# Performance work log

Measured on AMD Instinct MI355X. Metric: run time of the kernel, lower is better.

Reference implementation:

```python
import jax, jax.numpy as jnp
import numpy as np

B, NUM_OBJECTS, NUM_ATTRS, T = 8, 128, 4, 12
MAX_CONCEPTS, EMBED_DIM, IDENTITY_DIM, ATTENTION_DIM, HIDDEN_DIM = 2048, 128, 64, 64, 256
OP_MODE, OP_INSERT, OP_TRANSFER = 0, 1, 2


def setup_inputs() -> dict:
    key = jax.random.key(0)
    ks = jax.random.split(key, 24)
    def rn(k, shape, s=0.05):
        return s * jax.random.normal(k, shape, dtype=jnp.float32)
    return {
        'scene': jax.random.randint(ks[0], (B, NUM_OBJECTS, NUM_ATTRS), 0, MAX_CONCEPTS - 1),
        'program_op': jax.random.randint(ks[1], (B, T), 0, 3),
        'program_arg': jax.random.randint(ks[2], (B, T), 0, MAX_CONCEPTS),
        'attr_emb_in': rn(ks[3], (MAX_CONCEPTS, EMBED_DIM)),
        'attr_emb_out': rn(ks[4], (MAX_CONCEPTS, EMBED_DIM)),
        'attr_emb_id': rn(ks[5], (MAX_CONCEPTS, IDENTITY_DIM)),
        'concept_emb_in': rn(ks[6], (MAX_CONCEPTS, EMBED_DIM)),
        'concept_emb_out': rn(ks[7], (MAX_CONCEPTS, EMBED_DIM)),
        'concept_emb_id': rn(ks[8], (MAX_CONCEPTS, IDENTITY_DIM)),
        'embed_init': rn(ks[9], (EMBED_DIM,)),
        'identity_init': rn(ks[10], (IDENTITY_DIM,)),
        'attention_init': jnp.zeros((ATTENTION_DIM,), dtype=jnp.float32),
        'axon_w1': rn(ks[11], (HIDDEN_DIM, ATTENTION_DIM + IDENTITY_DIM)),
        'axon_b1': rn(ks[12], (HIDDEN_DIM,)),
        'axon_w2': rn(ks[13], (ATTENTION_DIM, HIDDEN_DIM)),
        'axon_b2': rn(ks[14], (ATTENTION_DIM,)),
        'meta_w1': rn(ks[15], (HIDDEN_DIM, EMBED_DIM + ATTENTION_DIM)),
        'meta_b1': rn(ks[16], (HIDDEN_DIM,)),
        'meta_w2': rn(ks[17], (ATTENTION_DIM, HIDDEN_DIM)),
        'meta_b2': rn(ks[18], (ATTENTION_DIM,)),
    }


def _mlp(x, w1, b1, w2, b2):
    # torch Linear convention: y = x @ W.T + b
    return jnp.maximum(x @ w1.T + b1, 0.0) @ w2.T + b2


def reference(scene, program_op, program_arg, attr_emb_in, attr_emb_out, attr_emb_id,
              concept_emb_in, concept_emb_out, concept_emb_id,
              embed_init, identity_init, attention_init,
              axon_w1, axon_b1, axon_w2, axon_b2,
              meta_w1, meta_b1, meta_w2, meta_b2):
    Bq, N, _ = scene.shape
    C = MAX_CONCEPTS + N  # dim_concept
    mask = (scene != -1).astype(jnp.float32)  # (B,N,A) non-background mask
    def embed_bg(E):
        return (E[scene + 1] * mask[..., None]).sum(2)  # (B,N,D)
    objects_in = embed_bg(attr_emb_in)
    objects_out = embed_bg(attr_emb_out)
    objects_id = embed_bg(attr_emb_id)

    rep = lambda w: jnp.broadcast_to(w[None], (Bq,) + w.shape)
    dendron = jnp.concatenate([rep(concept_emb_in), objects_in], 1)    # (B,C,E)
    axon = jnp.concatenate([rep(concept_emb_out), objects_out], 1)     # (B,C,E)
    identity = jnp.concatenate([rep(concept_emb_id), objects_id], 1)   # (B,C,Id)
    weight_matrix = jnp.einsum('bie,bje->bij', dendron, axon)           # (B,C,C)

    arguments = concept_emb_out[program_arg]                            # (B,T,E)
    is_mode = (program_op == OP_MODE).astype(jnp.float32)               # (B,T)
    is_insert = (program_op == OP_INSERT).astype(jnp.float32)
    is_transfer = (program_op == OP_TRANSFER).astype(jnp.float32)

    meta0 = jnp.broadcast_to(attention_init[None], (Bq, ATTENTION_DIM))
    att0 = jnp.broadcast_to(attention_init[None, None], (Bq, C, ATTENTION_DIM))

    def step(carry, xs):
        meta, attention = carry
        arg_i, m, ins, tr = xs  # (B,E), (B,), (B,), (B,)
        new_meta = _mlp(jnp.concatenate([meta, arg_i], 1), meta_w1, meta_b1, meta_w2, meta_b2)
        meta = m[:, None] * new_meta + (1.0 - m[:, None]) * meta
        # (arguments * axon).mean over embed dim -> (B,C)
        proj = jnp.einsum('be,bce->bc', arg_i, axon) / EMBED_DIM
        attention_insert = meta[:, None, :] * proj[:, :, None]          # (B,C,A)
        attended_weight = weight_matrix * attention.mean(2)[:, None, :] # (B,C,C)
        ia = jnp.concatenate([identity, attention], 2)                  # (B,C,Id+A)
        # (attended_weight[:,:,:,None] * ia[:,None]).mean(2) == matmul / C
        gathered = jnp.einsum('bij,bjd->bid', attended_weight, ia) / C  # (B,C,Id+A)
        attention_transfer = _mlp(gathered, axon_w1, axon_b1, axon_w2, axon_b2) + gathered[..., IDENTITY_DIM:]
        attention = attention + ins[:, None, None] * attention_insert + tr[:, None, None] * attention_transfer
        attention = jnp.clip(jnp.where(attention >= 0, attention, 0.01 * attention), -1.0, 2.0)
        return (meta, attention), (attention, attention_insert, attention_transfer)

    xs = (jnp.swapaxes(arguments, 0, 1), is_mode.T, is_insert.T, is_transfer.T)
    (meta, attention), (att_hist, ins_hist, trans_hist) = jax.lax.scan(step, (meta0, att0), xs)
    output_softmax = jax.nn.log_softmax(attention.mean(2), axis=1)  # (B,C)
    return (output_softmax, att_hist, ins_hist, trans_hist)
```

## Files before the change

### kernel.cpp

```cpp
#include <hip/hip_runtime.h>

#define B 8
#define NOBJ 128
#define NATTR 4
#define T 12
#define MC 2048
#define E 128
#define IDD 64
#define AD 64
#define HD 256
#define C 2176

typedef short s16x8 __attribute__((ext_vector_type(8)));
typedef float f32x4 __attribute__((ext_vector_type(4)));

__device__ inline unsigned short f2b(float f) {
  union { float f; unsigned u; } v; v.f = f;
  unsigned r = v.u + 0x7FFFu + ((v.u >> 16) & 1u);
  return (unsigned short)(r >> 16);
}
__device__ inline float b2f(unsigned short u) {
  union { unsigned u; float f; } v; v.u = ((unsigned)u) << 16;
  return v.f;
}

__device__ __forceinline__ void st_coh_u64(unsigned long long* p, unsigned long long v) {
  __hip_atomic_store(p, v, __ATOMIC_RELAXED, __HIP_MEMORY_SCOPE_AGENT);
}
__device__ __forceinline__ unsigned long long ld_coh_u64(const unsigned long long* p) {
  return __hip_atomic_load(p, __ATOMIC_RELAXED, __HIP_MEMORY_SCOPE_AGENT);
}
__device__ __forceinline__ void st_coh_u32(unsigned* p, unsigned v) {
  __hip_atomic_store(p, v, __ATOMIC_RELAXED, __HIP_MEMORY_SCOPE_AGENT);
}
__device__ __forceinline__ unsigned ld_coh_u32(const unsigned* p) {
  return __hip_atomic_load(p, __ATOMIC_RELAXED, __HIP_MEMORY_SCOPE_AGENT);
}

__device__ __forceinline__ int gidx(int r, int c) {
  return r * 128 + ((((c >> 3) ^ (r & 15)) << 3) | (c & 7));
}
__device__ __forceinline__ int hidx(int r, int c) {
  return r * 256 + ((((c >> 3) ^ (r & 15)) << 3) | (c & 7));
}
__device__ __forceinline__ int mtidx(int r, int c) {
  return r * 128 + ((((c >> 3) ^ (r & 15)) << 3) | (c & 7));
}

__global__ __launch_bounds__(256) void k_setup1(
    const int* __restrict__ scene,
    const float* __restrict__ aein, const float* __restrict__ aeout,
    const float* __restrict__ aeid,
    const float* __restrict__ cein, const float* __restrict__ ceout,
    const float* __restrict__ ceid,
    const float* __restrict__ aw1, const float* __restrict__ aw2,
    const float* __restrict__ mw1, const float* __restrict__ mw2,
    unsigned short* __restrict__ dendron_bf, float* __restrict__ axon,
    float* __restrict__ identity,
    unsigned short* __restrict__ w1_bf, unsigned short* __restrict__ w2_bf,
    float* __restrict__ mw1T, float* __restrict__ mw2T,
    unsigned* __restrict__ mflag) {
  int blk = blockIdx.x;
  int tid = threadIdx.x;
  if (blk < 4352) {
    int gid = blk * 2 + (tid >> 7);
    int e = tid & 127;
    int b = gid / C, j = gid % C;
    float din, dout, did = 0.f;
    if (j < MC) {
      din  = cein[j * E + e];
      dout = ceout[j * E + e];
      if (e < IDD) did = ceid[j * IDD + e];
    } else {
      int obj = j - MC;
      float sIn = 0.f, sOut = 0.f, sId = 0.f;
      for (int a = 0; a < NATTR; a++) {
        int s = scene[(b * NOBJ + obj) * NATTR + a];
        float m = (s != -1) ? 1.f : 0.f;
        int idx = s + 1;
        sIn  += aein[idx * E + e] * m;
        sOut += aeout[idx * E + e] * m;
        if (e < IDD) sId += aeid[idx * IDD + e] * m;
      }
      din = sIn; dout = sOut; did = sId;
    }
    dendron_bf[(size_t)gid * E + e] = f2b(din);
    axon[(size_t)gid * E + e] = dout;
    if (e < IDD) identity[(size_t)gid * IDD + e] = did;
  } else if (blk < 4544) {
    int i = (blk - 4352) * 256 + tid;
    if (i < HD * E)  w1_bf[i] = f2b(aw1[i]);
    if (i < AD * HD) w2_bf[i] = f2b(aw2[i]);
    if (i < 192 * HD) { int c = i / HD, k = i % HD; mw1T[c * HD + k] = mw1[k * 192 + c]; }
    if (i < HD * AD)  { int k = i / AD, a = i % AD; mw2T[k * AD + a] = mw2[a * HD + k]; }
  } else {
    if (tid < B * 16) mflag[tid] = 0u;
  }
}

__global__ __launch_bounds__(256) void k_setup2(
    const float* __restrict__ axon, const float* __restrict__ identity,
    const float* __restrict__ att_init,
    const int* __restrict__ prog_op, const int* __restrict__ prog_arg,
    const float* __restrict__ ceout,
    const float* __restrict__ mw1T, const float* __restrict__ mb1,
    const float* __restrict__ mw2T, const float* __restrict__ mb2,
    unsigned short* __restrict__ axonT, unsigned short* __restrict__ idT_g,
    unsigned short* __restrict__ siaT, float* __restrict__ att_g,
    float* __restrict__ meta_all, float* __restrict__ proj_all) {
  int blk = blockIdx.x;
  int tid = threadIdx.x;
  if (blk < 272) {
    int b = blk / 34, jc = blk % 34;
    int j0 = jc * 64;
    __shared__ float ax[64][129];
    __shared__ float idb[64][65];
    int lane = tid & 63, lr = lane & 15;
    float s = att_init[lane];
    s += __shfl_xor(s, 1, 64);  s += __shfl_xor(s, 2, 64);
    s += __shfl_xor(s, 4, 64);  s += __shfl_xor(s, 8, 64);
    s += __shfl_xor(s, 16, 64); s += __shfl_xor(s, 32, 64);
    float am0 = s * (1.f / AD);
    for (int i = tid; i < 64 * 128; i += 256) {
      int j = i >> 7, e = i & 127;
      ax[j][e] = axon[(size_t)(b * C + j0 + j) * E + e];
    }
    for (int i = tid; i < 64 * 64; i += 256) {
      int j = i >> 6, d = i & 63;
      idb[j][d] = identity[(size_t)(b * C + j0 + j) * IDD + d];
    }
    __syncthreads();
    for (int i = tid; i < 128 * 64; i += 256) {
      int e = i >> 6, jj = i & 63;
      axonT[(size_t)(b * E + e) * C + j0 + jj] = f2b(ax[jj][e]);
    }
    for (int i = tid; i < 64 * 64; i += 256) {
      int d = i >> 6, jj = i & 63;
      idT_g[(size_t)(b * 64 + d) * C + j0 + jj] = f2b(idb[jj][d]);
      siaT[(size_t)(b * 128 + d) * C + j0 + jj] = f2b(idb[jj][d] * am0);
      siaT[(size_t)(b * 128 + 64 + d) * C + j0 + jj] = f2b(att_init[d] * am0);
    }
    {
      float* ag = att_g + (size_t)blk * 4096 + tid * 16;
      #pragma unroll
      for (int n = 0; n < 4; n++) {
        float v0 = att_init[n * 16 + lr];
        #pragma unroll
        for (int v = 0; v < 4; v++) ag[n * 4 + v] = v0;
      }
    }
  } else if (blk < 280) {
    int b = blk - 272;
    __shared__ float x[192];
    __shared__ float h[HD];
    __shared__ float meta[AD];
    if (tid < AD) meta[tid] = att_init[tid];
    __syncthreads();
    for (int t = 0; t < T; t++) {
      int arg = prog_arg[b * T + t];
      if (tid < AD) x[tid] = meta[tid];
      else if (tid < 192) x[tid] = ceout[arg * E + (tid - 64)];
      __syncthreads();
      float s = mb1[tid];
      for (int c = 0; c < 192; c++) s += x[c] * mw1T[c * HD + tid];
      h[tid] = fmaxf(s, 0.f);
      __syncthreads();
      if (tid < AD) {
        float o = mb2[tid];
        for (int k = 0; k < HD; k++) o += h[k] * mw2T[k * AD + tid];
        float m = (prog_op[b * T + t] == 0) ? 1.f : 0.f;
        float nm = m * o + (1.f - m) * meta[tid];
        meta[tid] = nm;
        meta_all[(t * B + b) * AD + tid] = nm;
      }
      __syncthreads();
    }
  } else {
    int gid = (blk - 280) * 4 + (tid >> 6);
    int lane = tid & 63;
    int b = gid / C, i = gid % C;
    float a0 = axon[(size_t)gid * E + lane];
    float a1 = axon[(size_t)gid * E + 64 + lane];
    for (int t = 0; t < T; t++) {
      int arg = prog_arg[b * T + t];
      float p = a0 * ceout[arg * E + lane] + a1 * ceout[arg * E + 64 + lane];
      for (int off = 1; off < 64; off <<= 1) p += __shfl_xor(p, off, 64);
      if (lane == 0) proj_all[(size_t)(t * B + b) * C + i] = p * (1.f / E);
    }
  }
}

__global__ __launch_bounds__(256) void k_step(
    int t,
    const unsigned short* __restrict__ dendron_bf,
    const unsigned short* __restrict__ axonT,
    const unsigned short* __restrict__ idT_g,
    const unsigned short* __restrict__ siaT_in,
    const unsigned short* __restrict__ w1_bf, const float* __restrict__ b1g,
    const unsigned short* __restrict__ w2_bf, const float* __restrict__ b2g,
    const float* __restrict__ proj_all, const float* __restrict__ meta_all,
    const int* __restrict__ prog_op,
    unsigned long long* __restrict__ Mt64,
    float* __restrict__ att_g, unsigned short* __restrict__ siaT_out,
    float* __restrict__ rowmean,
    float* __restrict__ att_hist, float* __restrict__ ins_hist,
    float* __restrict__ trans_hist,
    unsigned* __restrict__ mflag) {
  const int blk = blockIdx.x;
  const int b = blk / 34, ch = blk % 34, j0 = ch * 64;
  const int tid = threadIdx.x;
  const int w = tid >> 6, lane = tid & 63, lr = lane & 15, lg = lane >> 4;

  __shared__ unsigned short smem[24576];
  __shared__ float am_l[64];
  unsigned short* g_l = smem;
  unsigned short* mt  = smem + 8192;
  unsigned short* h_l = smem + 8192;
  float* mred = (float*)smem;

  const f32x4 z = {0.f, 0.f, 0.f, 0.f};
  const unsigned ph = (unsigned)(t + 1);

  float att[4][4];
  {
    const f32x4* ag = (const f32x4*)(att_g + (size_t)blk * 4096 + tid * 16);
    #pragma unroll
    for (int n = 0; n < 4; n++) {
      f32x4 v4 = ag[n];
      #pragma unroll
      for (int v = 0; v < 4; v++) att[n][v] = v4[v];
    }
  }

  if (ch < 16) {
    int d0 = (ch >> 2) * 32, e0 = (ch & 3) * 32;
    const unsigned short* ap0 = siaT_in + (size_t)(b * 128 + d0 + lr) * C + w * 544 + lg * 8;
    const unsigned short* ap1 = ap0 + (size_t)16 * C;
    const unsigned short* bp0 = axonT + (size_t)(b * E + e0 + lr) * C + w * 544 + lg * 8;
    const unsigned short* bp1 = bp0 + (size_t)16 * C;
    f32x4 a00 = z, a01 = z, a10 = z, a11 = z;
    #pragma unroll 4
    for (int kk = 0; kk < 17; kk++) {
      int k0 = kk * 32;
      s16x8 A0 = *(const s16x8*)(ap0 + k0);
      s16x8 A1 = *(const s16x8*)(ap1 + k0);
      s16x8 B0 = *(const s16x8*)(bp0 + k0);
      s16x8 B1 = *(const s16x8*)(bp1 + k0);
      a00 = __builtin_amdgcn_mfma_f32_16x16x32_bf16(A0, B0, a00, 0, 0, 0);
      a01 = __builtin_amdgcn_mfma_f32_16x16x32_bf16(A0, B1, a01, 0, 0, 0);
      a10 = __builtin_amdgcn_mfma_f32_16x16x32_bf16(A1, B0, a10, 0, 0, 0);
      a11 = __builtin_amdgcn_mfma_f32_16x16x32_bf16(A1, B1, a11, 0, 0, 0);
    }
    #pragma unroll
    for (int v = 0; v < 4; v++) {
      mred[(w * 32 + lg * 4 + v) * 33 + lr]          = a00[v];
      mred[(w * 32 + lg * 4 + v) * 33 + 16 + lr]     = a01[v];
      mred[(w * 32 + 16 + lg * 4 + v) * 33 + lr]     = a10[v];
      mred[(w * 32 + 16 + lg * 4 + v) * 33 + 16 + lr] = a11[v];
    }
    __syncthreads();
    {
      int r = tid >> 3, c = (tid & 7) * 4;
      float s0 = 0.f, s1 = 0.f, s2 = 0.f, s3 = 0.f;
      #pragma unroll
      for (int w4 = 0; w4 < 4; w4++) {
        const float* p = &mred[(w4 * 32 + r) * 33 + c];
        s0 += p[0]; s1 += p[1]; s2 += p[2]; s3 += p[3];
      }
      unsigned long long pk = (unsigned long long)f2b(s0)
                            | ((unsigned long long)f2b(s1) << 16)
                            | ((unsigned long long)f2b(s2) << 32)
                            | ((unsigned long long)f2b(s3) << 48);
      st_coh_u64(Mt64 + (((size_t)(b * 128 + d0 + r) * 128) + e0 + c) / 4, pk);
    }
    asm volatile("s_waitcnt vmcnt(0)" ::: "memory");
    __syncthreads();
    if (tid == 0) st_coh_u32(mflag + b * 16 + ch, ph);
  }
  if (tid < 16) {
    while (ld_coh_u32(mflag + b * 16 + tid) < ph) __builtin_amdgcn_s_sleep(1);
  }
  __syncthreads();
  {
    const unsigned long long* mtp = Mt64 + (size_t)b * 4096;
    #pragma unroll
    for (int k = 0; k < 16; k++) {
      int idx = tid + k * 256;
      unsigned long long v = ld_coh_u64(mtp + idx);
      int r = idx >> 5, c4 = (idx & 31) * 4;
      *(unsigned long long*)&mt[mtidx(r, c4)] = v;
    }
  }
  __syncthreads();
  {
    s16x8 afr[4];
    #pragma unroll
    for (int ke = 0; ke < 4; ke++)
      afr[ke] = *(const s16x8*)(dendron_bf + (size_t)(b * C + j0 + w * 16 + lr) * E + ke * 32 + lg * 8);
    #pragma unroll
    for (int n = 0; n < 8; n++) {
      f32x4 acc = z;
      #pragma unroll
      for (int ke = 0; ke < 4; ke++) {
        s16x8 bf = *(const s16x8*)&mt[mtidx(n * 16 + lr, ke * 32 + lg * 8)];
        acc = __builtin_amdgcn_mfma_f32_16x16x32_bf16(afr[ke], bf, acc, 0, 0, 0);
      }
      #pragma unroll
      for (int v = 0; v < 4; v++)
        g_l[gidx(w * 16 + lg * 4 + v, n * 16 + lr)] = f2b(acc[v] * (1.f / C));
    }
  }
  __syncthreads();
  {
    s16x8 gf[4];
    #pragma unroll
    for (int kd = 0; kd < 4; kd++)
      gf[kd] = *(const s16x8*)&g_l[gidx(w * 16 + lr, kd * 32 + lg * 8)];
    #pragma unroll
    for (int n = 0; n < 16; n++) {
      f32x4 acc = z;
      #pragma unroll
      for (int kd = 0; kd < 4; kd++) {
        s16x8 bf = *(const s16x8*)(w1_bf + (size_t)(n * 16 + lr) * E + kd * 32 + lg * 8);
        acc = __builtin_amdgcn_mfma_f32_16x16x32_bf16(gf[kd], bf, acc, 0, 0, 0);
      }
      float b1v = b1g[n * 16 + lr];
      #pragma unroll
      for (int v = 0; v < 4; v++)
        h_l[hidx(w * 16 + lg * 4 + v, n * 16 + lr)] = f2b(fmaxf(acc[v] + b1v, 0.f));
    }
  }
  __syncthreads();
  {
    s16x8 hf[8];
    #pragma unroll
    for (int kk = 0; kk < 8; kk++)
      hf[kk] = *(const s16x8*)&h_l[hidx(w * 16 + lr, kk * 32 + lg * 8)];
    int op = prog_op[b * T + t];
    float insF = (op == 1) ? 1.f : 0.f, trF = (op == 2) ? 1.f : 0.f;
    float projv[4];
    #pragma unroll
    for (int v = 0; v < 4; v++)
      projv[v] = proj_all[(size_t)(t * B + b) * C + j0 + w * 16 + lg * 4 + v];
    #pragma unroll
    for (int n = 0; n < 4; n++) {
      f32x4 acc = z;
      #pragma unroll
      for (int kk = 0; kk < 8; kk++) {
        s16x8 bf = *(const s16x8*)(w2_bf + (size_t)(n * 16 + lr) * HD + kk * 32 + lg * 8);
        acc = __builtin_amdgcn_mfma_f32_16x16x32_bf16(hf[kk], bf, acc, 0, 0, 0);
      }
      int a = n * 16 + lr;
      float b2v = b2g[a];
      float meta_a = meta_all[(size_t)(t * B + b) * AD + a];
      #pragma unroll
      for (int v = 0; v < 4; v++) {
        int row = lg * 4 + v;
        int i = j0 + w * 16 + row;
        float transfer = acc[v] + b2v + b2f(g_l[gidx(w * 16 + row, 64 + a)]);
        float insert = meta_a * projv[v];
        float attv = att[n][v] + insF * insert + trF * transfer;
        attv = (attv >= 0.f) ? attv : 0.01f * attv;
        attv = fminf(fmaxf(attv, -1.f), 2.f);
        att[n][v] = attv;
        size_t hi = (((size_t)t * B + b) * C + i) * AD + a;
        __builtin_nontemporal_store(attv, att_hist + hi);
        __builtin_nontemporal_store(insert, ins_hist + hi);
        __builtin_nontemporal_store(transfer, trans_hist + hi);
      }
    }
  }
  float amr[4];
  {
    float s[4];
    #pragma unroll
    for (int v = 0; v < 4; v++) s[v] = att[0][v] + att[1][v] + att[2][v] + att[3][v];
    #pragma unroll
    for (int v = 0; v < 4; v++) {
      s[v] += __shfl_xor(s[v], 1, 64);
      s[v] += __shfl_xor(s[v], 2, 64);
      s[v] += __shfl_xor(s[v], 4, 64);
      s[v] += __shfl_xor(s[v], 8, 64);
      amr[v] = s[v] * (1.f / AD);
    }
    if (lr == 0) {
      #pragma unroll
      for (int v = 0; v < 4; v++) {
        am_l[w * 16 + lg * 4 + v] = amr[v];
        rowmean[(size_t)b * C + j0 + w * 16 + lg * 4 + v] = amr[v];
      }
    }
  }
  {
    f32x4* ag = (f32x4*)(att_g + (size_t)blk * 4096 + tid * 16);
    #pragma unroll
    for (int n = 0; n < 4; n++) {
      f32x4 v4;
      #pragma unroll
      for (int v = 0; v < 4; v++) v4[v] = att[n][v];
      ag[n] = v4;
      unsigned long long pk = 0;
      #pragma unroll
      for (int v = 0; v < 4; v++)
        pk |= (unsigned long long)f2b(att[n][v] * amr[v]) << (16 * v);
      *(unsigned long long*)(siaT_out + (size_t)(b * 128 + 64 + n * 16 + lr) * C + j0 + w * 16 + lg * 4) = pk;
    }
  }
  __syncthreads();
  #pragma unroll
  for (int k = 0; k < 2; k++) {
    int idx = tid + k * 256;
    int d = idx >> 3, part = idx & 7;
    int j = part * 8;
    s16x8 iv = *(const s16x8*)(idT_g + (size_t)(b * 64 + d) * C + j0 + j);
    s16x8 ov;
    #pragma unroll
    for (int m = 0; m < 8; m++)
      ov[m] = (short)f2b(b2f((unsigned short)iv[m]) * am_l[j + m]);
    *(s16x8*)(siaT_out + (size_t)(b * 128 + d) * C + j0 + j) = ov;
  }
}

__global__ void k_softmax(const float* __restrict__ rowmean, float* __restrict__ out) {
  int b = blockIdx.x;
  __shared__ float am[C];
  __shared__ float red[256];
  int tid = threadIdx.x;
  for (int i = tid; i < C; i += 256) am[i] = rowmean[(size_t)b * C + i];
  __syncthreads();
  float mx = -1e30f;
  for (int i = tid; i < C; i += 256) mx = fmaxf(mx, am[i]);
  red[tid] = mx; __syncthreads();
  for (int s = 128; s > 0; s >>= 1) { if (tid < s) red[tid] = fmaxf(red[tid], red[tid + s]); __syncthreads(); }
  mx = red[0]; __syncthreads();
  float sm = 0.f;
  for (int i = tid; i < C; i += 256) sm += expf(am[i] - mx);
  red[tid] = sm; __syncthreads();
  for (int s = 128; s > 0; s >>= 1) { if (tid < s) red[tid] += red[tid + s]; __syncthreads(); }
  float lse = logf(red[0]) + mx;
  for (int i = tid; i < C; i += 256) out[(size_t)b * C + i] = am[i] - lse;
}

extern "C" void kernel_launch(void* const* d_in, const int* in_sizes, int n_in,
                              void* d_out, int out_size, void* d_ws, size_t ws_size,
                              hipStream_t stream) {
  const int* scene     = (const int*)d_in[0];
  const int* prog_op   = (const int*)d_in[1];
  const int* prog_arg  = (const int*)d_in[2];
  const float* aein    = (const float*)d_in[3];
  const float* aeout   = (const float*)d_in[4];
  const float* aeid    = (const float*)d_in[5];
  const float* cein    = (const float*)d_in[6];
  const float* ceout   = (const float*)d_in[7];
  const float* ceid    = (const float*)d_in[8];
  const float* att_init = (const float*)d_in[11];
  const float* aw1 = (const float*)d_in[12];
  const float* ab1 = (const float*)d_in[13];
  const float* aw2 = (const float*)d_in[14];
  const float* ab2 = (const float*)d_in[15];
  const float* mw1 = (const float*)d_in[16];
  const float* mb1 = (const float*)d_in[17];
  const float* mw2 = (const float*)d_in[18];
  const float* mb2 = (const float*)d_in[19];

  char* ws = (char*)d_ws;
  size_t off = 0;
  auto carve = [&](size_t bytes) { char* p = ws + off; off += (bytes + 255) & ~(size_t)255; return p; };
  float* axon      = (float*)carve((size_t)B * C * E * 4);
  float* identity  = (float*)carve((size_t)B * C * IDD * 4);
  float* proj_all  = (float*)carve((size_t)T * B * C * 4);
  float* meta_all  = (float*)carve((size_t)T * B * AD * 4);
  float* mw1T      = (float*)carve((size_t)192 * HD * 4);
  float* mw2T      = (float*)carve((size_t)HD * AD * 4);
  float* rowmean   = (float*)carve((size_t)B * C * 4);
  float* att_g     = (float*)carve((size_t)272 * 4096 * 4);
  unsigned short* dendron_bf = (unsigned short*)carve((size_t)B * C * E * 2);
  unsigned short* axonT      = (unsigned short*)carve((size_t)B * E * C * 2);
  unsigned short* idT_g      = (unsigned short*)carve((size_t)B * 64 * C * 2);
  unsigned short* siaT       = (unsigned short*)carve((size_t)B * 128 * C * 2);
  unsigned long long* Mt64   = (unsigned long long*)carve((size_t)B * 4096 * 8);
  unsigned short* w1_bf      = (unsigned short*)carve((size_t)HD * E * 2);
  unsigned short* w2_bf      = (unsigned short*)carve((size_t)AD * HD * 2);
  unsigned*       mflag      = (unsigned*)carve(1024);

  float* out_sm     = (float*)d_out;
  float* att_hist   = out_sm + B * C;
  float* ins_hist   = att_hist + (size_t)T * B * C * AD;
  float* trans_hist = ins_hist + (size_t)T * B * C * AD;

  k_setup1<<<dim3(4545), dim3(256), 0, stream>>>(scene, aein, aeout, aeid, cein, ceout, ceid,
                                                 aw1, aw2, mw1, mw2,
                                                 dendron_bf, axon, identity,
                                                 w1_bf, w2_bf, mw1T, mw2T, mflag);
  k_setup2<<<dim3(1368), dim3(256), 0, stream>>>(axon, identity, att_init,
                                                 prog_op, prog_arg, ceout,
                                                 mw1T, mb1, mw2T, mb2,
                                                 axonT, idT_g, siaT, att_g,
                                                 meta_all, proj_all);
  for (int t = 0; t < T; t++) {
    k_step<<<dim3(272), dim3(256), 0, stream>>>(t, dendron_bf, axonT, idT_g, siaT,
                                                w1_bf, ab1, w2_bf, ab2,
                                                proj_all, meta_all, prog_op,
                                                Mt64, att_g, siaT, rowmean,
                                                att_hist, ins_hist, trans_hist, mflag);
  }
  k_softmax<<<dim3(B), dim3(256), 0, stream>>>(rowmean, out_sm);
}
```

Before: 655.4 us.

## Fuse three scan steps per launch with inter-block flag synchronization

Replaces the twelve per-step kernel launches with four launches, each running three consecutive time steps. Between steps, blocks publish their siaT slices and wait on per-batch completion flags instead of relying on kernel boundaries. Intermediate buffers are triple-buffered and attention state stays in registers across steps. This cuts launch overhead and register/global reloads, at the cost of spin-waits that need all 272 blocks co-resident and extra coherent stores.

```diff
diff --git a/kernel.cpp b/kernel.cpp
--- a/kernel.cpp
+++ b/kernel.cpp
@@ -26,9 +26,6 @@
 
 __device__ __forceinline__ void st_coh_u64(unsigned long long* p, unsigned long long v) {
   __hip_atomic_store(p, v, __ATOMIC_RELAXED, __HIP_MEMORY_SCOPE_AGENT);
-}
-__device__ __forceinline__ unsigned long long ld_coh_u64(const unsigned long long* p) {
-  return __hip_atomic_load(p, __ATOMIC_RELAXED, __HIP_MEMORY_SCOPE_AGENT);
 }
 __device__ __forceinline__ void st_coh_u32(unsigned* p, unsigned v) {
   __hip_atomic_store(p, v, __ATOMIC_RELAXED, __HIP_MEMORY_SCOPE_AGENT);
@@ -59,7 +56,7 @@
     float* __restrict__ identity,
     unsigned short* __restrict__ w1_bf, unsigned short* __restrict__ w2_bf,
     float* __restrict__ mw1T, float* __restrict__ mw2T,
-    unsigned* __restrict__ mflag) {
+    unsigned* __restrict__ flags) {
   int blk = blockIdx.x;
   int tid = threadIdx.x;
   if (blk < 4352) {
@@ -94,7 +91,7 @@
     if (i < 192 * HD) { int c = i / HD, k = i % HD; mw1T[c * HD + k] = mw1[k * 192 + c]; }
     if (i < HD * AD)  { int k = i / AD, a = i % AD; mw2T[k * AD + a] = mw2[a * HD + k]; }
   } else {
-    if (tid < B * 16) mflag[tid] = 0u;
+    for (int i = tid; i < 512; i += 256) flags[i] = 0u;
   }
 }
 
@@ -190,22 +187,24 @@
   }
 }
 
-__global__ __launch_bounds__(256) void k_step(
-    int t,
+__global__ __launch_bounds__(256, 2) void k_grp(
+    int t0,
     const unsigned short* __restrict__ dendron_bf,
     const unsigned short* __restrict__ axonT,
     const unsigned short* __restrict__ idT_g,
-    const unsigned short* __restrict__ siaT_in,
+    const unsigned short* __restrict__ sIN,
+    unsigned short* __restrict__ sM1,
+    unsigned short* __restrict__ sM2,
+    unsigned short* __restrict__ sOUT,
     const unsigned short* __restrict__ w1_bf, const float* __restrict__ b1g,
     const unsigned short* __restrict__ w2_bf, const float* __restrict__ b2g,
     const float* __restrict__ proj_all, const float* __restrict__ meta_all,
     const int* __restrict__ prog_op,
     unsigned long long* __restrict__ Mt64,
-    float* __restrict__ att_g, unsigned short* __restrict__ siaT_out,
-    float* __restrict__ rowmean,
+    float* __restrict__ att_g, float* __restrict__ rowmean,
     float* __restrict__ att_hist, float* __restrict__ ins_hist,
     float* __restrict__ trans_hist,
-    unsigned* __restrict__ mflag) {
+    unsigned* __restrict__ mflag, unsigned* __restrict__ cflag) {
   const int blk = blockIdx.x;
   const int b = blk / 34, ch = blk % 34, j0 = ch * 64;
   const int tid = threadIdx.x;
@@ -216,10 +215,10 @@
   unsigned short* g_l = smem;
   unsigned short* mt  = smem + 8192;
   unsigned short* h_l = smem + 8192;
-  float* mred = (float*)smem;
 
   const f32x4 z = {0.f, 0.f, 0.f, 0.f};
-  const unsigned ph = (unsigned)(t + 1);
+  const unsigned short* srcs[3] = {sIN, sM1, sM2};
+  unsigned short* dsts[3] = {sM1, sM2, sOUT};
 
   float att[4][4];
   {
@@ -231,163 +230,209 @@
       for (int v = 0; v < 4; v++) att[n][v] = v4[v];
     }
   }
-
-  if (ch < 16) {
-    int d0 = (ch >> 2) * 32, e0 = (ch & 3) * 32;
-    const unsigned short* ap0 = siaT_in + (size_t)(b * 128 + d0 + lr) * C + w * 544 + lg * 8;
-    const unsigned short* ap1 = ap0 + (size_t)16 * C;
-    const unsigned short* bp0 = axonT + (size_t)(b * E + e0 + lr) * C + w * 544 + lg * 8;
-    const unsigned short* bp1 = bp0 + (size_t)16 * C;
-    f32x4 a00 = z, a01 = z, a10 = z, a11 = z;
-    #pragma unroll 4
-    for (int kk = 0; kk < 17; kk++) {
-      int k0 = kk * 32;
-      s16x8 A0 = *(const s16x8*)(ap0 + k0);
-      s16x8 A1 = *(const s16x8*)(ap1 + k0);
-      s16x8 B0 = *(const s16x8*)(bp0 + k0);
-      s16x8 B1 = *(const s16x8*)(bp1 + k0);
-      a00 = __builtin_amdgcn_mfma_f32_16x16x32_bf16(A0, B0, a00, 0, 0, 0);
-      a01 = __builtin_amdgcn_mfma_f32_16x16x32_bf16(A0, B1, a01, 0, 0, 0);
-      a10 = __builtin_amdgcn_mfma_f32_16x16x32_bf16(A1, B0, a10, 0, 0, 0);
-      a11 = __builtin_amdgcn_mfma_f32_16x16x32_bf16(A1, B1, a11, 0, 0, 0);
-    }
-    #pragma unroll
-    for (int v = 0; v < 4; v++) {
-      mred[(w * 32 + lg * 4 + v) * 33 + lr]          = a00[v];
-      mred[(w * 32 + lg * 4 + v) * 33 + 16 + lr]     = a01[v];
-      mred[(w * 32 + 16 + lg * 4 + v) * 33 + lr]     = a10[v];
-      mred[(w * 32 + 16 + lg * 4 + v) * 33 + 16 + lr] = a11[v];
+  s16x8 afr[4];
+  #pragma unroll
+  for (int ke = 0; ke < 4; ke++)
+    afr[ke] = *(const s16x8*)(dendron_bf + (size_t)(b * C + j0 + w * 16 + lr) * E + ke * 32 + lg * 8);
+
+  for (int sub = 0; sub < 3; sub++) {
+    const int t = t0 + sub;
+    const unsigned short* sia_src = srcs[sub];
+    unsigned long long* MtS = Mt64 + (size_t)sub * (B * 4096);
+    if (ch < 16) {
+      if (sub > 0) {
+        if (tid < 34) {
+          while (ld_coh_u32(cflag + b * 34 + tid) < (unsigned)t) __builtin_amdgcn_s_sleep(2);
+        }
+      }
+      __syncthreads();
+      int d0 = (ch >> 2) * 32, e0 = (ch & 3) * 32;
+      const unsigned short* ap0 = sia_src + (size_t)(b * 128 + d0 + lr) * C + w * 544 + lg * 8;
+      const unsigned short* ap1 = ap0 + (size_t)16 * C;
+      const unsigned short* bp0 = axonT + (size_t)(b * E + e0 + lr) * C + w * 544 + lg * 8;
+      const unsigned short* bp1 = bp0 + (size_t)16 * C;
+      f32x4 a00 = z, a01 = z, a10 = z, a11 = z;
+      #pragma unroll 4
+      for (int kk = 0; kk < 17; kk++) {
+        int k0 = kk * 32;
+        s16x8 A0 = *(const s16x8*)(ap0 + k0);
+        s16x8 A1 = *(const s16x8*)(ap1 + k0);
+        s16x8 B0 = *(const s16x8*)(bp0 + k0);
+        s16x8 B1 = *(const s16x8*)(bp1 + k0);
+        a00 = __builtin_amdgcn_mfma_f32_16x16x32_bf16(A0, B0, a00, 0, 0, 0);
+        a01 = __builtin_amdgcn_mfma_f32_16x16x32_bf16(A0, B1, a01, 0, 0, 0);
+        a10 = __builtin_amdgcn_mfma_f32_16x16x32_bf16(A1, B0, a10, 0, 0, 0);
+        a11 = __builtin_amdgcn_mfma_f32_16x16x32_bf16(A1, B1, a11, 0, 0, 0);
+      }
+      float* mred = (float*)smem;
+      #pragma unroll
+      for (int v = 0; v < 4; v++) {
+        mred[(w * 32 + lg * 4 + v) * 33 + lr]           = a00[v];
+        mred[(w * 32 + lg * 4 + v) * 33 + 16 + lr]      = a01[v];
+        mred[(w * 32 + 16 + lg * 4 + v) * 33 + lr]      = a10[v];
+        mred[(w * 32 + 16 + lg * 4 + v) * 33 + 16 + lr] = a11[v];
+      }
+      __syncthreads();
+      {
+        int r = tid >> 3, c = (tid & 7) * 4;
+        float s0 = 0.f, s1 = 0.f, s2 = 0.f, s3 = 0.f;
+        #pragma unroll
+        for (int w4 = 0; w4 < 4; w4++) {
+          const float* p = &mred[(w4 * 32 + r) * 33 + c];
+          s0 += p[0]; s1 += p[1]; s2 += p[2]; s3 += p[3];
+        }
+        unsigned long long pk = (unsigned long long)f2b(s0)
+                              | ((unsigned long long)f2b(s1) << 16)
+                              | ((unsigned long long)f2b(s2) << 32)
+                              | ((unsigned long long)f2b(s3) << 48);
+        st_coh_u64(MtS + (((size_t)(b * 128 + d0 + r) * 128) + e0 + c) / 4, pk);
+      }
+      asm volatile("s_waitcnt vmcnt(0)" ::: "memory");
+      __syncthreads();
+      if (tid == 0) st_coh_u32(mflag + b * 16 + ch, (unsigned)(t + 1));
+    }
+    if (tid < 16) {
+      while (ld_coh_u32(mflag + b * 16 + tid) < (unsigned)(t + 1)) __builtin_amdgcn_s_sleep(2);
     }
     __syncthreads();
     {
-      int r = tid >> 3, c = (tid & 7) * 4;
-      float s0 = 0.f, s1 = 0.f, s2 = 0.f, s3 = 0.f;
-      #pragma unroll
-      for (int w4 = 0; w4 < 4; w4++) {
-        const float* p = &mred[(w4 * 32 + r) * 33 + c];
-        s0 += p[0]; s1 += p[1]; s2 += p[2]; s3 += p[3];
-      }
-      unsigned long long pk = (unsigned long long)f2b(s0)
-                            | ((unsigned long long)f2b(s1) << 16)
-                            | ((unsigned long long)f2b(s2) << 32)
-                            | ((unsigned long long)f2b(s3) << 48);
-      st_coh_u64(Mt64 + (((size_t)(b * 128 + d0 + r) * 128) + e0 + c) / 4, pk);
-    }
-    asm volatile("s_waitcnt vmcnt(0)" ::: "memory");
+      const unsigned long long* mtp = MtS + (size_t)b * 4096;
+      #pragma unroll
+      for (int k = 0; k < 16; k++) {
+        int idx = tid + k * 256;
+        unsigned long long v = mtp[idx];
+        int r = idx >> 5, c4 = (idx & 31) * 4;
+        *(unsigned long long*)&mt[mtidx(r, c4)] = v;
+      }
+    }
     __syncthreads();
-    if (tid == 0) st_coh_u32(mflag + b * 16 + ch, ph);
-  }
-  if (tid < 16) {
-    while (ld_coh_u32(mflag + b * 16 + tid) < ph) __builtin_amdgcn_s_sleep(1);
-  }
-  __syncthreads();
-  {
-    const unsigned long long* mtp = Mt64 + (size_t)b * 4096;
-    #pragma unroll
-    for (int k = 0; k < 16; k++) {
-      int idx = tid + k * 256;
-      unsigned long long v = ld_coh_u64(mtp + idx);
-      int r = idx >> 5, c4 = (idx & 31) * 4;
-      *(unsigned long long*)&mt[mtidx(r, c4)] = v;
-    }
-  }
-  __syncthreads();
-  {
-    s16x8 afr[4];
-    #pragma unroll
-    for (int ke = 0; ke < 4; ke++)
-      afr[ke] = *(const s16x8*)(dendron_bf + (size_t)(b * C + j0 + w * 16 + lr) * E + ke * 32 + lg * 8);
-    #pragma unroll
-    for (int n = 0; n < 8; n++) {
-      f32x4 acc = z;
-      #pragma unroll
-      for (int ke = 0; ke < 4; ke++) {
-        s16x8 bf = *(const s16x8*)&mt[mtidx(n * 16 + lr, ke * 32 + lg * 8)];
-        acc = __builtin_amdgcn_mfma_f32_16x16x32_bf16(afr[ke], bf, acc, 0, 0, 0);
-      }
+    {
+      #pragma unroll
+      for (int n = 0; n < 8; n++) {
+        f32x4 a2 = z;
+        #pragma unroll
+        for (int ke = 0; ke < 4; ke++) {
+          s16x8 bf = *(const s16x8*)&mt[mtidx(n * 16 + lr, ke * 32 + lg * 8)];
+          a2 = __builtin_amdgcn_mfma_f32_16x16x32_bf16(afr[ke], bf, a2, 0, 0, 0);
+        }
+        #pragma unroll
+        for (int v = 0; v < 4; v++)
+          g_l[gidx(w * 16 + lg * 4 + v, n * 16 + lr)] = f2b(a2[v] * (1.f / C));
+      }
+    }
+    __syncthreads();
+    {
+      s16x8 gf[4];
+      #pragma unroll
+      for (int kd = 0; kd < 4; kd++)
+        gf[kd] = *(const s16x8*)&g_l[gidx(w * 16 + lr, kd * 32 + lg * 8)];
+      #pragma unroll
+      for (int n = 0; n < 16; n++) {
+        f32x4 a2 = z;
+        #pragma unroll
+        for (int kd = 0; kd < 4; kd++) {
+          s16x8 bf = *(const s16x8*)(w1_bf + (size_t)(n * 16 + lr) * E + kd * 32 + lg * 8);
+          a2 = __builtin_amdgcn_mfma_f32_16x16x32_bf16(gf[kd], bf, a2, 0, 0, 0);
+        }
+        float b1v = b1g[n * 16 + lr];
+        #pragma unroll
+        for (int v = 0; v < 4; v++)
+          h_l[hidx(w * 16 + lg * 4 + v, n * 16 + lr)] = f2b(fmaxf(a2[v] + b1v, 0.f));
+      }
+    }
+    __syncthreads();
+    {
+      s16x8 hf[8];
+      #pragma unroll
+      for (int kk = 0; kk < 8; kk++)
+        hf[kk] = *(const s16x8*)&h_l[hidx(w * 16 + lr, kk * 32 + lg * 8)];
+      int op = prog_op[b * T + t];
+      float insF = (op == 1) ? 1.f : 0.f, trF = (op == 2) ? 1.f : 0.f;
+      float projv[4];
       #pragma unroll
       for (int v = 0; v < 4; v++)
-        g_l[gidx(w * 16 + lg * 4 + v, n * 16 + lr)] = f2b(acc[v] * (1.f / C));
-    }
-  }
-  __syncthreads();
-  {
-    s16x8 gf[4];
-    #pragma unroll
-    for (int kd = 0; kd < 4; kd++)
-      gf[kd] = *(const s16x8*)&g_l[gidx(w * 16 + lr, kd * 32 + lg * 8)];
-    #pragma unroll
-    for (int n = 0; n < 16; n++) {
-      f32x4 acc = z;
-      #pragma unroll
-      for (int kd = 0; kd < 4; kd++) {
-        s16x8 bf = *(const s16x8*)(w1_bf + (size_t)(n * 16 + lr) * E + kd * 32 + lg * 8);
-        acc = __builtin_amdgcn_mfma_f32_16x16x32_bf16(gf[kd], bf, acc, 0, 0, 0);
-      }
-      float b1v = b1g[n * 16 + lr];
-      #pragma unroll
-      for (int v = 0; v < 4; v++)
-        h_l[hidx(w * 16 + lg * 4 + v, n * 16 + lr)] = f2b(fmaxf(acc[v] + b1v, 0.f));
-    }
-  }
-  __syncthreads();
-  {
-    s16x8 hf[8];
-    #pragma unroll
-    for (int kk = 0; kk < 8; kk++)
-      hf[kk] = *(const s16x8*)&h_l[hidx(w * 16 + lr, kk * 32 + lg * 8)];
-    int op = prog_op[b * T + t];
-    float insF = (op == 1) ? 1.f : 0.f, trF = (op == 2) ? 1.f : 0.f;
-    float projv[4];
-    #pragma unroll
-    for (int v = 0; v < 4; v++)
-      projv[v] = proj_all[(size_t)(t * B + b) * C + j0 + w * 16 + lg * 4 + v];
-    #pragma unroll
-    for (int n = 0; n < 4; n++) {
-      f32x4 acc = z;
-      #pragma unroll
-      for (int kk = 0; kk < 8; kk++) {
-        s16x8 bf = *(const s16x8*)(w2_bf + (size_t)(n * 16 + lr) * HD + kk * 32 + lg * 8);
-        acc = __builtin_amdgcn_mfma_f32_16x16x32_bf16(hf[kk], bf, acc, 0, 0, 0);
-      }
-      int a = n * 16 + lr;
-      float b2v = b2g[a];
-      float meta_a = meta_all[(size_t)(t * B + b) * AD + a];
+        projv[v] = proj_all[(size_t)(t * B + b) * C + j0 + w * 16 + lg * 4 + v];
+      #pragma unroll
+      for (int n = 0; n < 4; n++) {
+        f32x4 a2 = z;
+        #pragma unroll
+        for (int kk = 0; kk < 8; kk++) {
+          s16x8 bf = *(const s16x8*)(w2_bf + (size_t)(n * 16 + lr) * HD + kk * 32 + lg * 8);
+          a2 = __builtin_amdgcn_mfma_f32_16x16x32_bf16(hf[kk], bf, a2, 0, 0, 0);
+        }
+        int a = n * 16 + lr;
+        float b2v = b2g[a];
+        float meta_a = meta_all[(size_t)(t * B + b) * AD + a];
+        #pragma unroll
+        for (int v = 0; v < 4; v++) {
+          int row = lg * 4 + v;
+          int i = j0 + w * 16 + row;
+          float transfer = a2[v] + b2v + b2f(g_l[gidx(w * 16 + row, 64 + a)]);
+          float insert = meta_a * projv[v];
+          float attv = att[n][v] + insF * insert + trF * transfer;
+          attv = (attv >= 0.f) ? attv : 0.01f * attv;
+          attv = fminf(fmaxf(attv, -1.f), 2.f);
+          att[n][v] = attv;
+          size_t hi = (((size_t)t * B + b) * C + i) * AD + a;
+          __builtin_nontemporal_store(attv, att_hist + hi);
+          __builtin_nontemporal_store(insert, ins_hist + hi);
+          __builtin_nontemporal_store(transfer, trans_hist + hi);
+        }
+      }
+    }
+    float amr[4];
+    {
+      float s[4];
+      #pragma unroll
+      for (int v = 0; v < 4; v++) s[v] = att[0][v] + att[1][v] + att[2][v] + att[3][v];
       #pragma unroll
       for (int v = 0; v < 4; v++) {
-        int row = lg * 4 + v;
-        int i = j0 + w * 16 + row;
-        float transfer = acc[v] + b2v + b2f(g_l[gidx(w * 16 + row, 64 + a)]);
-        float insert = meta_a * projv[v];
-        float attv = att[n][v] + insF * insert + trF * transfer;
-        attv = (attv >= 0.f) ? attv : 0.01f * attv;
-        attv = fminf(fmaxf(attv, -1.f), 2.f);
-        att[n][v] = attv;
-        size_t hi = (((size_t)t * B + b) * C + i) * AD + a;
-        __builtin_nontemporal_store(attv, att_hist + hi);
-        __builtin_nontemporal_store(insert, ins_hist + hi);
-        __builtin_nontemporal_store(transfer, trans_hist + hi);
-      }
-    }
-  }
-  float amr[4];
-  {
-    float s[4];
-    #pragma unroll
-    for (int v = 0; v < 4; v++) s[v] = att[0][v] + att[1][v] + att[2][v] + att[3][v];
-    #pragma unroll
-    for (int v = 0; v < 4; v++) {
-      s[v] += __shfl_xor(s[v], 1, 64);
-      s[v] += __shfl_xor(s[v], 2, 64);
-      s[v] += __shfl_xor(s[v], 4, 64);
-      s[v] += __shfl_xor(s[v], 8, 64);
-      amr[v] = s[v] * (1.f / AD);
-    }
-    if (lr == 0) {
-      #pragma unroll
-      for (int v = 0; v < 4; v++) {
-        am_l[w * 16 + lg * 4 + v] = amr[v];
-        rowmean[(size_t)b * C + j0 + w * 16 + lg * 4 + v] = amr[v];
+        s[v] += __shfl_xor(s[v], 1, 64);
+        s[v] += __shfl_xor(s[v], 2, 64);
+        s[v] += __shfl_xor(s[v], 4, 64);
+        s[v] += __shfl_xor(s[v], 8, 64);
+        amr[v] = s[v] * (1.f / AD);
+      }
+      if (lr == 0) {
+        #pragma unroll
+        for (int v = 0; v < 4; v++) am_l[w * 16 + lg * 4 + v] = amr[v];
+      }
+    }
+    if (t < T - 1) {
+      unsigned short* s_dst = dsts[sub];
+      #pragma unroll
+      for (int n = 0; n < 4; n++) {
+        unsigned long long pk = 0;
+        #pragma unroll
+        for (int v = 0; v < 4; v++)
+          pk |= (unsigned long long)f2b(att[n][v] * amr[v]) << (16 * v);
+        st_coh_u64((unsigned long long*)(s_dst + (size_t)(b * 128 + 64 + n * 16 + lr) * C + j0 + w * 16 + lg * 4), pk);
+      }
+      __syncthreads();
+      #pragma unroll
+      for (int k2 = 0; k2 < 2; k2++) {
+        int idx = tid + k2 * 256;
+        int d = idx >> 3, part = idx & 7;
+        int j = part * 8;
+        s16x8 iv = *(const s16x8*)(idT_g + (size_t)(b * 64 + d) * C + j0 + j);
+        union { s16x8 v; unsigned long long u[2]; } ov;
+        #pragma unroll
+        for (int m = 0; m < 8; m++)
+          ov.v[m] = (short)f2b(b2f((unsigned short)iv[m]) * am_l[j + m]);
+        unsigned long long* dst = (unsigned long long*)(s_dst + (size_t)(b * 128 + d) * C + j0 + j);
+        st_coh_u64(dst, ov.u[0]);
+        st_coh_u64(dst + 1, ov.u[1]);
+      }
+      if (sub < 2) {
+        asm volatile("s_waitcnt vmcnt(0)" ::: "memory");
+        __syncthreads();
+        if (tid == 0) st_coh_u32(cflag + b * 34 + ch, (unsigned)(t + 1));
+      }
+    } else {
+      if (lr == 0) {
+        #pragma unroll
+        for (int v = 0; v < 4; v++)
+          rowmean[(size_t)b * C + j0 + w * 16 + lg * 4 + v] = amr[v];
       }
     }
   }
@@ -399,25 +444,7 @@
       #pragma unroll
       for (int v = 0; v < 4; v++) v4[v] = att[n][v];
       ag[n] = v4;
-      unsigned long long pk = 0;
-      #pragma unroll
-      for (int v = 0; v < 4; v++)
-        pk |= (unsigned long long)f2b(att[n][v] * amr[v]) << (16 * v);
-      *(unsigned long long*)(siaT_out + (size_t)(b * 128 + 64 + n * 16 + lr) * C + j0 + w * 16 + lg * 4) = pk;
-    }
-  }
-  __syncthreads();
-  #pragma unroll
-  for (int k = 0; k < 2; k++) {
-    int idx = tid + k * 256;
-    int d = idx >> 3, part = idx & 7;
-    int j = part * 8;
-    s16x8 iv = *(const s16x8*)(idT_g + (size_t)(b * 64 + d) * C + j0 + j);
-    s16x8 ov;
-    #pragma unroll
-    for (int m = 0; m < 8; m++)
-      ov[m] = (short)f2b(b2f((unsigned short)iv[m]) * am_l[j + m]);
-    *(s16x8*)(siaT_out + (size_t)(b * 128 + d) * C + j0 + j) = ov;
+    }
   }
 }
 
@@ -477,11 +504,16 @@
   unsigned short* dendron_bf = (unsigned short*)carve((size_t)B * C * E * 2);
   unsigned short* axonT      = (unsigned short*)carve((size_t)B * E * C * 2);
   unsigned short* idT_g      = (unsigned short*)carve((size_t)B * 64 * C * 2);
-  unsigned short* siaT       = (unsigned short*)carve((size_t)B * 128 * C * 2);
-  unsigned long long* Mt64   = (unsigned long long*)carve((size_t)B * 4096 * 8);
+  unsigned short* siaA       = (unsigned short*)carve((size_t)B * 128 * C * 2);
+  unsigned short* siaB       = (unsigned short*)carve((size_t)B * 128 * C * 2);
+  unsigned short* siaM1      = (unsigned short*)carve((size_t)B * 128 * C * 2);
+  unsigned short* siaM2      = (unsigned short*)carve((size_t)B * 128 * C * 2);
+  unsigned long long* Mt64   = (unsigned long long*)carve((size_t)3 * B * 4096 * 8);
   unsigned short* w1_bf      = (unsigned short*)carve((size_t)HD * E * 2);
   unsigned short* w2_bf      = (unsigned short*)carve((size_t)AD * HD * 2);
-  unsigned*       mflag      = (unsigned*)carve(1024);
+  unsigned*       flags      = (unsigned*)carve(2048);
+  unsigned*       mflag = flags;
+  unsigned*       cflag = flags + 128;
 
   float* out_sm     = (float*)d_out;
   float* att_hist   = out_sm + B * C;
@@ -491,18 +523,22 @@
   k_setup1<<<dim3(4545), dim3(256), 0, stream>>>(scene, aein, aeout, aeid, cein, ceout, ceid,
                                                  aw1, aw2, mw1, mw2,
                                                  dendron_bf, axon, identity,
-                                                 w1_bf, w2_bf, mw1T, mw2T, mflag);
+                                                 w1_bf, w2_bf, mw1T, mw2T, flags);
   k_setup2<<<dim3(1368), dim3(256), 0, stream>>>(axon, identity, att_init,
                                                  prog_op, prog_arg, ceout,
                                                  mw1T, mb1, mw2T, mb2,
-                                                 axonT, idT_g, siaT, att_g,
+                                                 axonT, idT_g, siaA, att_g,
                                                  meta_all, proj_all);
-  for (int t = 0; t < T; t++) {
-    k_step<<<dim3(272), dim3(256), 0, stream>>>(t, dendron_bf, axonT, idT_g, siaT,
-                                                w1_bf, ab1, w2_bf, ab2,
-                                                proj_all, meta_all, prog_op,
-                                                Mt64, att_g, siaT, rowmean,
-                                                att_hist, ins_hist, trans_hist, mflag);
+  for (int g = 0; g < 4; g++) {
+    const unsigned short* sin = (g & 1) ? siaB : siaA;
+    unsigned short* sout      = (g & 1) ? siaA : siaB;
+    k_grp<<<dim3(272), dim3(256), 0, stream>>>(3 * g, dendron_bf, axonT, idT_g,
+                                               sin, siaM1, siaM2, sout,
+                                               w1_bf, ab1, w2_bf, ab2,
+                                               proj_all, meta_all, prog_op,
+                                               Mt64, att_g, rowmean,
+                                               att_hist, ins_hist, trans_hist,
+                                               mflag, cflag);
   }
   k_softmax<<<dim3(B), dim3(256), 0, stream>>>(rowmean, out_sm);
 }
```

New measurement: 1.248 ms. +90.5%, slower.
